# Performance work log

Hardware: AMD Instinct MI355X
Metric: run time of the kernel (lower is better)

Reference implementation:

```python
import jax, jax.numpy as jnp
import numpy as np

DIST = 22.63      # __init__ kwarg `dist` (cdist threshold)
DS_SIZE = 80      # hard-coded Downsample result_size in LeafBranchFunc
LOG_CLAMP = 100.0 # torch BCE clamps log terms at -100


def _cdist(x):
    # x: [B,N,F] -> pairwise euclidean distances [B,N,N]
    sq = jnp.sum(x * x, axis=-1)
    d2 = sq[:, :, None] + sq[:, None, :] - 2.0 * jnp.einsum('bnf,bmf->bnm', x, x)
    return jnp.sqrt(jnp.maximum(d2, 0.0))


@jax.jit
def _cluster(point_features):
    """Faithful port of Cluster.forward: threshold cdist, then the strictly
    sequential greedy label stamping with a single global next_label counter."""
    adj = _cdist(point_features) < DIST  # [B,N,N] bool
    N = adj.shape[1]
    idx = jnp.arange(N)

    def row_step(carry, xs):
        labels, nxt = carry
        row, i = xs
        cur = labels[i]
        new = jnp.where(cur == 0, nxt, cur)
        nxt = jnp.where(cur == 0, nxt + 1, nxt)
        labels = labels.at[i].set(new)
        labels = jnp.where(row, new, labels)  # stamp all thresholded neighbors
        return (labels, nxt), None

    def batch_step(nxt, adj_b):
        (labels, nxt), _ = jax.lax.scan(row_step, (jnp.zeros(N, jnp.int32), nxt), (adj_b, idx))
        return nxt, labels

    _, labels = jax.lax.scan(batch_step, jnp.int32(1), adj)  # sequential over batch: shared counter
    return labels  # [B,N] int32


def _classify(pts, W1, b1, W2, b2, W3, b3):
    # pts: [K,80,3] -> P(class 1) per cluster, PointNet-lite classifier + softmax
    h = jax.nn.relu(pts @ W1 + b1)       # [K,80,64]
    h = jax.nn.relu(h @ W2 + b2)         # [K,80,128]
    g = jnp.max(h, axis=1)               # [K,128] global max pool
    logits = g @ W3 + b3                 # [K,2]
    return jax.nn.softmax(logits, axis=-1)[:, 1]


def setup_inputs() -> dict:
    key = jax.random.key(0)
    ks = jax.random.split(key, 8)
    B, N, F = 4, 4096, 256
    return {
        'point_features': jax.random.normal(ks[0], (B, N, F), jnp.float32),
        'points': jax.random.normal(ks[1], (B, N, 3), jnp.float32),
        'W1': jax.random.normal(ks[2], (3, 64), jnp.float32) * 0.5,
        'b1': jnp.zeros((64,), jnp.float32),
        'W2': jax.random.normal(ks[3], (64, 128), jnp.float32) * 0.1,
        'b2': jnp.zeros((128,), jnp.float32),
        'W3': jax.random.normal(ks[4], (128, 2), jnp.float32) * 0.1,
        'b3': jnp.zeros((2,), jnp.float32),
    }


def reference(point_features, points, W1, b1, W2, b2, W3, b3):
    labels = np.asarray(_cluster(point_features))  # [B,N]; cluster ids are data-dependent
    points_np = np.asarray(points)
    rng = np.random.RandomState(0)  # Downsample uses np.random.choice with replacement
    total = jnp.float32(0.0)
    for b in range(labels.shape[0]):
        ds = []
        for c in np.unique(labels[b]):
            cp = points_np[b][labels[b] == c]                    # [M,3] points of this cluster
            sel = rng.choice(cp.shape[0], DS_SIZE, replace=True)  # random downsample to 80
            ds.append(cp[sel])
        ds = jnp.asarray(np.stack(ds), dtype=jnp.float32)        # [K,80,3]
        p = jnp.nan_to_num(_classify(ds, W1, b1, W2, b2, W3, b3))
        # binary_cross_entropy with all-ones targets: mean(-log p), log clamped at -100
        loss = jnp.mean(jnp.minimum(-jnp.log(p), LOG_CLAMP))
        total = total + loss
    return total
```

## Files before the change

### kernel.cpp

```cpp
#include <hip/hip_runtime.h>
#include <math.h>
#include <stdint.h>
#include <stdlib.h>

constexpr int B_ = 4, N_ = 4096, F_ = 256;
constexpr int DS = 80;
constexpr int MAXC = 16384;
constexpr int RAWBLKS = 16;
constexpr int RAWN = 624 * RAWBLKS;

namespace {
struct RawStream {
  unsigned* buf = nullptr;
  RawStream() {
    unsigned mt[624];
    mt[0] = 0u;
    for (int i = 1; i < 624; ++i)
      mt[i] = 1812433253u * (mt[i - 1] ^ (mt[i - 1] >> 30)) + (unsigned)i;
    if (hipHostMalloc((void**)&buf, (size_t)(RAWN + 624) * 4, 0) != hipSuccess || !buf)
      buf = (unsigned*)malloc((size_t)(RAWN + 624) * 4);
    for (int blk = 0; blk < RAWBLKS; ++blk) {
      for (int i = 0; i < 624; ++i) {
        unsigned y = (mt[i] & 0x80000000u) | (mt[(i + 1) % 624] & 0x7fffffffu);
        mt[i] = mt[(i + 397) % 624] ^ (y >> 1) ^ ((y & 1u) ? 0x9908b0dfu : 0u);
      }
      for (int i = 0; i < 624; ++i) {
        unsigned y = mt[i];
        y ^= y >> 11; y ^= (y << 7) & 0x9d2c5680u; y ^= (y << 15) & 0xefc60000u; y ^= y >> 18;
        buf[blk * 624 + i] = y;
      }
    }
    for (int i = 0; i < 624; ++i) buf[RAWN + i] = mt[i];
  }
};
RawStream g_raw;
}

__global__ __launch_bounds__(256) void pre_kernel(const float* __restrict__ x,
                                                  float* __restrict__ sq,
                                                  int* __restrict__ arrivals) {
  const int blk = blockIdx.x, tid = threadIdx.x;
  const int i = blk * 256 + tid;
  float4 v = ((const float4*)x)[i];
  float s = v.x * v.x + v.y * v.y + v.z * v.z + v.w * v.w;
  for (int off = 32; off > 0; off >>= 1) s += __shfl_down(s, off);
  if ((tid & 63) == 0) sq[blk * 4 + (tid >> 6)] = s;
  if (blk == 0 && tid == 0) arrivals[0] = 0;
}

__device__ __forceinline__ int scan_dir(const float* __restrict__ xb,
                                        const float* __restrict__ sqb,
                                        float4 a0, float4 a1, float4 a2, float4 a3,
                                        double sqi, int jhi, int jlo, int gl, int g) {
  if (jhi < jlo) return -1;
  const double THR2D = (double)22.63f * (double)22.63f;
  int j0 = jhi;
  int cjA = j0 - g;     if (cjA < jlo) cjA = jlo;
  int cjB = j0 - 4 - g; if (cjB < jlo) cjB = jlo;
  const float4* rA = (const float4*)(xb + (size_t)cjA * F_);
  const float4* rB = (const float4*)(xb + (size_t)cjB * F_);
  float4 cA0 = rA[gl], cA1 = rA[gl + 16], cA2 = rA[gl + 32], cA3 = rA[gl + 48];
  float4 cB0 = rB[gl], cB1 = rB[gl + 16], cB2 = rB[gl + 32], cB3 = rB[gl + 48];

  while (j0 >= jlo) {
    const int jn = j0 - 8;
    int nA = jn - g;     if (nA < jlo) nA = jlo;
    int nB = jn - 4 - g; if (nB < jlo) nB = jlo;
    const float4* rnA = (const float4*)(xb + (size_t)nA * F_);
    const float4* rnB = (const float4*)(xb + (size_t)nB * F_);
    float4 pA0 = rnA[gl], pA1 = rnA[gl + 16], pA2 = rnA[gl + 32], pA3 = rnA[gl + 48];
    float4 pB0 = rnB[gl], pB1 = rnB[gl + 16], pB2 = rnB[gl + 32], pB3 = rnB[gl + 48];

    float sA = 0.f;
    sA += a0.x * cA0.x + a0.y * cA0.y + a0.z * cA0.z + a0.w * cA0.w;
    sA += a1.x * cA1.x + a1.y * cA1.y + a1.z * cA1.z + a1.w * cA1.w;
    sA += a2.x * cA2.x + a2.y * cA2.y + a2.z * cA2.z + a2.w * cA2.w;
    sA += a3.x * cA3.x + a3.y * cA3.y + a3.z * cA3.z + a3.w * cA3.w;
    float sB = 0.f;
    sB += a0.x * cB0.x + a0.y * cB0.y + a0.z * cB0.z + a0.w * cB0.w;
    sB += a1.x * cB1.x + a1.y * cB1.y + a1.z * cB1.z + a1.w * cB1.w;
    sB += a2.x * cB2.x + a2.y * cB2.y + a2.z * cB2.z + a2.w * cB2.w;
    sB += a3.x * cB3.x + a3.y * cB3.y + a3.z * cB3.z + a3.w * cB3.w;
    sA += __shfl_xor(sA, 1); sA += __shfl_xor(sA, 2);
    sA += __shfl_xor(sA, 4); sA += __shfl_xor(sA, 8);
    sB += __shfl_xor(sB, 1); sB += __shfl_xor(sB, 2);
    sB += __shfl_xor(sB, 4); sB += __shfl_xor(sB, 8);

    bool okA = false, okB = false;
    const int mA = j0 - g, mB = j0 - 4 - g;
    if (mA >= jlo) {
      double d2 = sqi + (double)sqb[mA] - 2.0 * (double)sA;
      okA = d2 < THR2D;
    }
    if (mB >= jlo) {
      double d2 = sqi + (double)sqb[mB] - 2.0 * (double)sB;
      okB = d2 < THR2D;
    }
    unsigned long long balA = __ballot(okA);
    unsigned long long balB = __ballot(okB);
    if (balA) return j0 - ((__ffsll(balA) - 1) >> 4);
    if (balB) return j0 - 4 - ((__ffsll(balB) - 1) >> 4);
    cA0 = pA0; cA1 = pA1; cA2 = pA2; cA3 = pA3;
    cB0 = pB0; cB1 = pB1; cB2 = pB2; cB3 = pB3;
    j0 = jn;
  }
  return -1;
}

__global__ __launch_bounds__(256) void scan_kernel(const float* __restrict__ x,
                                                   const float* __restrict__ sq,
                                                   int* __restrict__ p,
                                                   int* __restrict__ q) {
  const int tid = threadIdx.x;
  const int w = tid >> 6, lane = tid & 63;
  const int bb = blockIdx.x & 3;
  const int rg = blockIdx.x >> 2;
  const int i = rg * 4 + w;
  const float* xb = x + (size_t)bb * N_ * F_;
  const float* sqb = sq + (size_t)bb * N_;
  const int gl = lane & 15, g = lane >> 4;

  const float4* ra = (const float4*)(xb + (size_t)i * F_);
  float4 a0 = ra[gl], a1 = ra[gl + 16], a2 = ra[gl + 32], a3 = ra[gl + 48];
  const double sqi = (double)sqb[i];

  const int qf = scan_dir(xb, sqb, a0, a1, a2, a3, sqi, N_ - 1, i + 1, gl, g);
  const int pf = scan_dir(xb, sqb, a0, a1, a2, a3, sqi, i - 1, 0, gl, g);

  if (lane == 0) {
    const size_t o = (size_t)bb * N_ + i;
    q[o] = (qf < 0) ? i : qf;
    p[o] = pf;
  }
}

__global__ __launch_bounds__(1024) void cluster_kernel(const int* __restrict__ p,
                                                       const int* __restrict__ q,
                                                       int* __restrict__ lab,
                                                       int* __restrict__ Karr, int* __restrict__ labs,
                                                       int* __restrict__ Msz) {
  const int b = blockIdx.x, tid = threadIdx.x;
  __shared__ int A[N_ + 1], Bb[N_], labS[N_];
  __shared__ int waveOff[17];
  __shared__ int runBase, chg;

  for (int k = tid; k < N_; k += 1024) {
    int pi = p[(size_t)b * N_ + k];
    A[k] = (pi < 0) ? k : pi;
  }
  __syncthreads();
  int* src = A; int* dst = Bb;
  for (int it = 0; it < 12; ++it) {
    if (tid == 0) chg = 0;
    __syncthreads();
    bool any = false;
    for (int k = tid; k < N_; k += 1024) {
      int v = src[src[k]];
      dst[k] = v;
      any |= (v != src[k]);
    }
    if (any) chg = 1;
    __syncthreads();
    int* t = src; src = dst; dst = t;
    if (!chg) break;
  }
  if (tid == 0) runBase = 0;
  __syncthreads();
  for (int base = 0; base < N_; base += 1024) {
    int i = base + tid;
    bool isR = (src[i] == i);
    unsigned long long bal = __ballot(isR);
    int lane = tid & 63, wid = tid >> 6;
    if (lane == 0) waveOff[wid] = __popcll(bal);
    __syncthreads();
    if (tid == 0) {
      int s = runBase;
      for (int w = 0; w < 16; ++w) { int t2 = waveOff[w]; waveOff[w] = s; s += t2; }
      waveOff[16] = s;
    }
    __syncthreads();
    int incl = __popcll(bal & (~0ull >> (63 - lane)));
    dst[i] = waveOff[wid] + incl;
    __syncthreads();
    if (tid == 0) runBase = waveOff[16];
    __syncthreads();
  }
  for (int j = tid; j < N_; j += 1024) {
    int qq = q[(size_t)b * N_ + j];
    int lv = dst[src[qq]];
    labS[j] = lv;
    lab[(size_t)b * N_ + j] = lv;
  }
  __syncthreads();

  int* cnt = A;
  for (int k = tid; k <= N_; k += 1024) cnt[k] = 0;
  __syncthreads();
  {
    const int lane = tid & 63;
    for (int j = tid; j < N_; j += 1024) {
      int v = labS[j];
      unsigned long long remM = ~0ull;
      while (remM) {
        int leader = __ffsll(remM) - 1;
        int lv = __shfl(v, leader);
        unsigned long long m = __ballot(v == lv);
        if (lane == leader) atomicAdd(&cnt[lv], __popcll(m));
        remM &= ~m;
      }
    }
  }
  __syncthreads();
  if (tid == 0) runBase = 0;
  __syncthreads();
  for (int base = 1; base <= N_; base += 1024) {
    int c = base + tid;
    bool m = (cnt[c] > 0);
    unsigned long long bal = __ballot(m);
    int lane = tid & 63, wid = tid >> 6;
    if (lane == 0) waveOff[wid] = __popcll(bal);
    __syncthreads();
    if (tid == 0) {
      int s = runBase;
      for (int w = 0; w < 16; ++w) { int t2 = waveOff[w]; waveOff[w] = s; s += t2; }
      waveOff[16] = s;
    }
    __syncthreads();
    if (m) {
      int pos = waveOff[wid] + __popcll(bal & ((1ull << lane) - 1));
      labs[(size_t)b * N_ + pos] = c;
      Msz[(size_t)b * N_ + pos] = cnt[c];
    }
    __syncthreads();
    if (tid == 0) runBase = waveOff[16];
    __syncthreads();
  }
  if (tid == 0) Karr[b] = runBase;
}

__device__ inline void mt_regen(unsigned* mt, unsigned* raw, int lane) {
  const int ph_s[3] = {0, 227, 454};
  const int ph_e[3] = {227, 454, 624};
#pragma unroll
  for (int ph = 0; ph < 3; ++ph) {
    const int s = ph_s[ph], e = ph_e[ph];
    unsigned aReg[4], bReg[4];
    const int niter = (e - s + 63) >> 6;
    for (int it = 0; it < niter; ++it) {
      int i = s + it * 64 + lane;
      if (i < e) { aReg[it] = mt[i]; bReg[it] = mt[(i + 1) % 624]; }
    }
    __syncthreads();
    for (int it = 0; it < niter; ++it) {
      int i = s + it * 64 + lane;
      if (i < e) {
        unsigned y = (aReg[it] & 0x80000000u) | (bReg[it] & 0x7fffffffu);
        mt[i] = mt[(i + 397) % 624] ^ (y >> 1) ^ ((y & 1u) ? 0x9908b0dfu : 0u);
      }
    }
    __syncthreads();
  }
  for (int it = 0; it < 10; ++it) {
    int i = it * 64 + lane;
    if (i < 624) {
      unsigned y = mt[i];
      y ^= y >> 11; y ^= (y << 7) & 0x9d2c5680u; y ^= (y << 15) & 0xefc60000u; y ^= y >> 18;
      raw[i] = y;
    }
  }
  __syncthreads();
}

__global__ __launch_bounds__(64) void rngsel_kernel(const int* __restrict__ Karr,
                                                    const int* __restrict__ Msz,
                                                    const unsigned* __restrict__ rawG,
                                                    const unsigned* __restrict__ mtSave,
                                                    int* __restrict__ sel, int* __restrict__ meta,
                                                    int* __restrict__ totK) {
  __shared__ int mszS[2048];
  __shared__ unsigned rawL[2048];
  __shared__ unsigned mtF[624];
  __shared__ unsigned rawF[624];
  const int lane = threadIdx.x;
  int pos = 0;
  int winBase = -100000;
  bool fb = false;
  int fpos = 0;
  int cid = 0;
  for (int b = 0; b < B_; ++b) {
    const int Kb = Karr[b];
    for (int k0 = 0; k0 < Kb; k0 += 2048) {
      const int nk = min(2048, Kb - k0);
      for (int i = lane; i < nk; i += 64) mszS[i] = Msz[(size_t)b * N_ + k0 + i];
      __syncthreads();
      for (int kk = 0; kk < nk; ++kk) {
        const int M = mszS[kk];
        if (lane == 0) meta[cid] = (b << 16) | (k0 + kk);
        if (M <= 1) {
          sel[cid * DS + lane] = 0;
          if (lane < DS - 64) sel[cid * DS + 64 + lane] = 0;
        } else {
          const unsigned rng = (unsigned)(M - 1);
          unsigned mask = rng;
          mask |= mask >> 1; mask |= mask >> 2; mask |= mask >> 4; mask |= mask >> 8; mask |= mask >> 16;
          int acc = 0;
          while (acc < DS) {
            unsigned v = 0xFFFFFFFFu;
            bool ok = false;
            int take;
            if (!fb && pos >= RAWN) {
              fb = true;
              for (int i = lane; i < 624; i += 64) mtF[i] = mtSave[i];
              __syncthreads();
              fpos = 624;
            }
            if (!fb) {
              if (pos + 64 > winBase + 2048) {
                winBase = pos;
                for (int i = lane; i < 2048; i += 64) rawL[i] = rawG[winBase + i];
                __syncthreads();
              }
              take = min(64, RAWN - pos);
              if (lane < take) { v = rawL[pos - winBase + lane] & mask; ok = (v <= rng); }
            } else {
              if (fpos == 624) { mt_regen(mtF, rawF, lane); fpos = 0; }
              take = min(64, 624 - fpos);
              if (lane < take) { v = rawF[fpos + lane] & mask; ok = (v <= rng); }
            }
            unsigned long long bal = __ballot(ok);
            int pre = __popcll(bal & ((1ull << lane) - 1ull));
            int tot = __popcll(bal);
            if (ok && acc + pre < DS) sel[cid * DS + acc + pre] = (int)v;
            int advance;
            if (acc + tot >= DS) {
              int need = DS - acc;
              bool win = ok && (pre + 1 == need);
              unsigned long long wb = __ballot(win);
              advance = __ffsll(wb);
              acc = DS;
            } else {
              advance = take;
              acc += tot;
            }
            if (fb) fpos += advance; else pos += advance;
          }
        }
        ++cid;
      }
      __syncthreads();
    }
  }
  if (lane == 0) totK[0] = cid;
}

__global__ __launch_bounds__(256) void classify_par_kernel(
    const float* __restrict__ points, const float* __restrict__ W1, const float* __restrict__ b1,
    const float* __restrict__ W2, const float* __restrict__ b2,
    const float* __restrict__ W3, const float* __restrict__ b3,
    const int* __restrict__ lab, const int* __restrict__ labs,
    const int* __restrict__ sel, const int* __restrict__ meta, const int* __restrict__ totK,
    const int* __restrict__ Karr, float* __restrict__ lossArr,
    int* __restrict__ arrivals, float* __restrict__ out) {
  __shared__ unsigned wordsS[128];
  __shared__ int prefS[128];
  __shared__ float pts[DS][3];
  __shared__ float h1[DS][64];
  __shared__ float W2s[64][128];
  __shared__ float gmax[128];
  __shared__ float accB[4];
  __shared__ int lastS;
  const int tid = threadIdx.x;
  int T = totK[0]; if (T > MAXC) T = MAXC;
  if ((int)blockIdx.x >= T) return;
  for (int k = tid; k < 64 * 128; k += 256) W2s[k >> 7][k & 127] = W2[k];

  for (int cid = blockIdx.x; cid < T; cid += gridDim.x) {
    const int mv = meta[cid];
    const int b = mv >> 16, k = mv & 0xFFFF;
    const int c = labs[(size_t)b * N_ + k];
    if (tid < 128) {
      unsigned wbits = 0;
      const int* lb = lab + (size_t)b * N_ + tid * 32;
      for (int s = 0; s < 32; ++s) wbits |= (lb[s] == c) ? (1u << s) : 0u;
      wordsS[tid] = wbits;
    }
    __syncthreads();
    if (tid == 0) {
      int s = 0;
      for (int w2 = 0; w2 < 128; ++w2) { prefS[w2] = s; s += __popc(wordsS[w2]); }
    }
    __syncthreads();
    if (tid < DS) {
      int r = sel[cid * DS + tid];
      int lo = 0, hi = 127;
      while (lo < hi) { int mid = (lo + hi + 1) >> 1; if (prefS[mid] <= r) lo = mid; else hi = mid - 1; }
      int rem = r - prefS[lo];
      unsigned wbits = wordsS[lo];
      int j = lo * 32;
      for (;;) {
        int bpos = __ffs(wbits) - 1;
        if (rem == 0) { j += bpos; break; }
        wbits &= wbits - 1; --rem;
      }
      pts[tid][0] = points[((size_t)b * N_ + j) * 3 + 0];
      pts[tid][1] = points[((size_t)b * N_ + j) * 3 + 1];
      pts[tid][2] = points[((size_t)b * N_ + j) * 3 + 2];
    }
    __syncthreads();
    for (int o = tid; o < DS * 64; o += 256) {
      int r = o >> 6, cc = o & 63;
      float v = pts[r][0] * W1[cc] + pts[r][1] * W1[64 + cc] + pts[r][2] * W1[128 + cc] + b1[cc];
      h1[r][cc] = fmaxf(v, 0.f);
    }
    __syncthreads();
    {
      const int cc = tid & 127, half = tid >> 7;
      const float b2c = b2[cc];
      float m = -1e30f;
      for (int r = half * 40; r < half * 40 + 40; ++r) {
        float a0 = 0.f, a1 = 0.f, a2 = 0.f, a3 = 0.f;
#pragma unroll
        for (int kk = 0; kk < 64; kk += 4) {
          a0 += h1[r][kk + 0] * W2s[kk + 0][cc];
          a1 += h1[r][kk + 1] * W2s[kk + 1][cc];
          a2 += h1[r][kk + 2] * W2s[kk + 2][cc];
          a3 += h1[r][kk + 3] * W2s[kk + 3][cc];
        }
        float acc = ((a0 + a1) + (a2 + a3)) + b2c;
        m = fmaxf(m, fmaxf(acc, 0.f));
      }
      if (half == 0) gmax[cc] = m;
      __syncthreads();
      if (half == 1) gmax[cc] = fmaxf(gmax[cc], m);
    }
    __syncthreads();
    if (tid == 0) {
      float l0 = b3[0], l1 = b3[1];
      for (int cc = 0; cc < 128; ++cc) { l0 += gmax[cc] * W3[cc * 2 + 0]; l1 += gmax[cc] * W3[cc * 2 + 1]; }
      float mx = fmaxf(l0, l1);
      float e0 = expf(l0 - mx), e1 = expf(l1 - mx);
      float p1 = e1 / (e0 + e1);
      if (isnan(p1)) p1 = 0.f;
      atomicExch(&lossArr[cid], fminf(-logf(p1), 100.f));
    }
    __syncthreads();
  }

  __threadfence();
  if (tid == 0) {
    const int active = min((int)gridDim.x, T);
    lastS = (atomicAdd(arrivals, 1) == active - 1) ? 1 : 0;
  }
  __syncthreads();
  if (!lastS) return;
  if (tid < 4) accB[tid] = 0.f;
  __syncthreads();
  float local[4] = {0.f, 0.f, 0.f, 0.f};
  for (int cid = tid; cid < T; cid += 256)
    local[meta[cid] >> 16] += atomicAdd(&lossArr[cid], 0.0f);
  for (int b = 0; b < 4; ++b) {
    float v = local[b];
    for (int off = 32; off > 0; off >>= 1) v += __shfl_down(v, off);
    if ((tid & 63) == 0) atomicAdd(&accB[b], v);
  }
  __syncthreads();
  if (tid == 0) {
    float tot = 0.f;
    for (int b = 0; b < 4; ++b) tot += accB[b] / (float)Karr[b];
    out[0] = tot;
  }
}

extern "C" void kernel_launch(void* const* d_in, const int* in_sizes, int n_in,
                              void* d_out, int out_size, void* d_ws, size_t ws_size,
                              hipStream_t stream) {
  const float* x      = (const float*)d_in[0];
  const float* points = (const float*)d_in[1];
  const float* W1 = (const float*)d_in[2];
  const float* b1 = (const float*)d_in[3];
  const float* W2 = (const float*)d_in[4];
  const float* b2 = (const float*)d_in[5];
  const float* W3 = (const float*)d_in[6];
  const float* b3 = (const float*)d_in[7];
  float* out = (float*)d_out;

  char* wsb = (char*)d_ws;
  size_t off = 0;
  auto carve = [&](size_t bytes) -> void* {
    void* r = wsb + off;
    off += (bytes + 255) & ~(size_t)255;
    return r;
  };
  float* sq      = (float*)carve((size_t)B_ * N_ * 4);
  int* p         = (int*)carve((size_t)B_ * N_ * 4);
  int* q         = (int*)carve((size_t)B_ * N_ * 4);
  int* lab       = (int*)carve((size_t)B_ * N_ * 4);
  int* labs      = (int*)carve((size_t)B_ * N_ * 4);
  int* Msz       = (int*)carve((size_t)B_ * N_ * 4);
  int* Karr      = (int*)carve(256);
  int* totK      = (int*)carve(256);
  int* arrivals  = (int*)carve(256);
  unsigned* rawG = (unsigned*)carve((size_t)(RAWN + 624 + 2048) * 4);
  unsigned* mtSave = rawG + RAWN;
  int* sel       = (int*)carve((size_t)MAXC * DS * 4);
  int* meta      = (int*)carve((size_t)MAXC * 4);
  float* lossArr = (float*)carve((size_t)MAXC * 4);
  (void)ws_size;

  hipMemcpyAsync(rawG, g_raw.buf, (size_t)(RAWN + 624) * 4,
                 hipMemcpyHostToDevice, stream);

  hipLaunchKernelGGL(pre_kernel, dim3(B_ * N_ * F_ / 1024), dim3(256), 0, stream,
                     x, sq, arrivals);
  hipLaunchKernelGGL(scan_kernel, dim3(B_ * N_ / 4), dim3(256), 0, stream, x, sq, p, q);
  hipLaunchKernelGGL(cluster_kernel, dim3(B_), dim3(1024), 0, stream,
                     p, q, lab, Karr, labs, Msz);
  hipLaunchKernelGGL(rngsel_kernel, dim3(1), dim3(64), 0, stream,
                     Karr, Msz, rawG, mtSave, sel, meta, totK);
  hipLaunchKernelGGL(classify_par_kernel, dim3(512), dim3(256), 0, stream,
                     points, W1, b1, W2, b2, W3, b3, lab, labs, sel, meta, totK,
                     Karr, lossArr, arrivals, out);
}
```

Before: 161.0 us.

## Bake MT19937 stream into device constant and split scan directions across waves

Replaces the per-call host-to-device copy of the precomputed Mersenne Twister raw stream with a constexpr-generated __device__ constant table, which removes a memcpy from each invocation. It also doubles the scan_kernel block to 512 threads so the forward (q) and backward (p) neighbour searches run on separate waves instead of one after the other in the same wave. This gives more parallelism and shortens the serial critical path per row. The cost is higher register and occupancy pressure per block, and a large constexpr evaluation at compile time.

```diff
diff --git a/kernel.cpp b/kernel.cpp
--- a/kernel.cpp
+++ b/kernel.cpp
@@ -9,32 +9,33 @@
 constexpr int RAWBLKS = 16;
 constexpr int RAWN = 624 * RAWBLKS;
 
-namespace {
-struct RawStream {
-  unsigned* buf = nullptr;
-  RawStream() {
-    unsigned mt[624];
-    mt[0] = 0u;
-    for (int i = 1; i < 624; ++i)
-      mt[i] = 1812433253u * (mt[i - 1] ^ (mt[i - 1] >> 30)) + (unsigned)i;
-    if (hipHostMalloc((void**)&buf, (size_t)(RAWN + 624) * 4, 0) != hipSuccess || !buf)
-      buf = (unsigned*)malloc((size_t)(RAWN + 624) * 4);
-    for (int blk = 0; blk < RAWBLKS; ++blk) {
-      for (int i = 0; i < 624; ++i) {
-        unsigned y = (mt[i] & 0x80000000u) | (mt[(i + 1) % 624] & 0x7fffffffu);
-        mt[i] = mt[(i + 397) % 624] ^ (y >> 1) ^ ((y & 1u) ? 0x9908b0dfu : 0u);
-      }
-      for (int i = 0; i < 624; ++i) {
-        unsigned y = mt[i];
-        y ^= y >> 11; y ^= (y << 7) & 0x9d2c5680u; y ^= (y << 15) & 0xefc60000u; y ^= y >> 18;
-        buf[blk * 624 + i] = y;
-      }
-    }
-    for (int i = 0; i < 624; ++i) buf[RAWN + i] = mt[i];
-  }
+struct MTData {
+  unsigned raw[RAWN];
+  unsigned save[624];
+  unsigned pad[2048];
 };
-RawStream g_raw;
-}
+
+constexpr MTData gen_mt() {
+  MTData d{};
+  unsigned mt[624]{};
+  mt[0] = 0u;
+  for (int i = 1; i < 624; ++i)
+    mt[i] = 1812433253u * (mt[i - 1] ^ (mt[i - 1] >> 30)) + (unsigned)i;
+  for (int blk = 0; blk < RAWBLKS; ++blk) {
+    for (int i = 0; i < 624; ++i) {
+      unsigned y = (mt[i] & 0x80000000u) | (mt[(i + 1) % 624] & 0x7fffffffu);
+      mt[i] = mt[(i + 397) % 624] ^ (y >> 1) ^ ((y & 1u) ? 0x9908b0dfu : 0u);
+    }
+    for (int i = 0; i < 624; ++i) {
+      unsigned y = mt[i];
+      y ^= y >> 11; y ^= (y << 7) & 0x9d2c5680u; y ^= (y << 15) & 0xefc60000u; y ^= y >> 18;
+      d.raw[blk * 624 + i] = y;
+    }
+  }
+  for (int i = 0; i < 624; ++i) d.save[i] = mt[i];
+  return d;
+}
+__device__ const MTData d_mt = gen_mt();
 
 __global__ __launch_bounds__(256) void pre_kernel(const float* __restrict__ x,
                                                   float* __restrict__ sq,
@@ -107,7 +108,7 @@
   return -1;
 }
 
-__global__ __launch_bounds__(256) void scan_kernel(const float* __restrict__ x,
+__global__ __launch_bounds__(512) void scan_kernel(const float* __restrict__ x,
                                                    const float* __restrict__ sq,
                                                    int* __restrict__ p,
                                                    int* __restrict__ q) {
@@ -115,7 +116,8 @@
   const int w = tid >> 6, lane = tid & 63;
   const int bb = blockIdx.x & 3;
   const int rg = blockIdx.x >> 2;
-  const int i = rg * 4 + w;
+  const int i = rg * 4 + (w & 3);
+  const bool qmode = (w >> 2) == 0;
   const float* xb = x + (size_t)bb * N_ * F_;
   const float* sqb = sq + (size_t)bb * N_;
   const int gl = lane & 15, g = lane >> 4;
@@ -124,13 +126,13 @@
   float4 a0 = ra[gl], a1 = ra[gl + 16], a2 = ra[gl + 32], a3 = ra[gl + 48];
   const double sqi = (double)sqb[i];
 
-  const int qf = scan_dir(xb, sqb, a0, a1, a2, a3, sqi, N_ - 1, i + 1, gl, g);
-  const int pf = scan_dir(xb, sqb, a0, a1, a2, a3, sqi, i - 1, 0, gl, g);
+  const int f = qmode ? scan_dir(xb, sqb, a0, a1, a2, a3, sqi, N_ - 1, i + 1, gl, g)
+                      : scan_dir(xb, sqb, a0, a1, a2, a3, sqi, i - 1, 0, gl, g);
 
   if (lane == 0) {
     const size_t o = (size_t)bb * N_ + i;
-    q[o] = (qf < 0) ? i : qf;
-    p[o] = pf;
+    if (qmode) q[o] = (f < 0) ? i : f;
+    else       p[o] = f;
   }
 }
 
@@ -273,8 +275,6 @@
 
 __global__ __launch_bounds__(64) void rngsel_kernel(const int* __restrict__ Karr,
                                                     const int* __restrict__ Msz,
-                                                    const unsigned* __restrict__ rawG,
-                                                    const unsigned* __restrict__ mtSave,
                                                     int* __restrict__ sel, int* __restrict__ meta,
                                                     int* __restrict__ totK) {
   __shared__ int mszS[2048];
@@ -310,14 +310,14 @@
             int take;
             if (!fb && pos >= RAWN) {
               fb = true;
-              for (int i = lane; i < 624; i += 64) mtF[i] = mtSave[i];
+              for (int i = lane; i < 624; i += 64) mtF[i] = d_mt.save[i];
               __syncthreads();
               fpos = 624;
             }
             if (!fb) {
               if (pos + 64 > winBase + 2048) {
                 winBase = pos;
-                for (int i = lane; i < 2048; i += 64) rawL[i] = rawG[winBase + i];
+                for (int i = lane; i < 2048; i += 64) rawL[i] = d_mt.raw[winBase + i];
                 __syncthreads();
               }
               take = min(64, RAWN - pos);
@@ -500,23 +500,18 @@
   int* Karr      = (int*)carve(256);
   int* totK      = (int*)carve(256);
   int* arrivals  = (int*)carve(256);
-  unsigned* rawG = (unsigned*)carve((size_t)(RAWN + 624 + 2048) * 4);
-  unsigned* mtSave = rawG + RAWN;
   int* sel       = (int*)carve((size_t)MAXC * DS * 4);
   int* meta      = (int*)carve((size_t)MAXC * 4);
   float* lossArr = (float*)carve((size_t)MAXC * 4);
   (void)ws_size;
 
-  hipMemcpyAsync(rawG, g_raw.buf, (size_t)(RAWN + 624) * 4,
-                 hipMemcpyHostToDevice, stream);
-
   hipLaunchKernelGGL(pre_kernel, dim3(B_ * N_ * F_ / 1024), dim3(256), 0, stream,
                      x, sq, arrivals);
-  hipLaunchKernelGGL(scan_kernel, dim3(B_ * N_ / 4), dim3(256), 0, stream, x, sq, p, q);
+  hipLaunchKernelGGL(scan_kernel, dim3(B_ * N_ / 4), dim3(512), 0, stream, x, sq, p, q);
   hipLaunchKernelGGL(cluster_kernel, dim3(B_), dim3(1024), 0, stream,
                      p, q, lab, Karr, labs, Msz);
   hipLaunchKernelGGL(rngsel_kernel, dim3(1), dim3(64), 0, stream,
-                     Karr, Msz, rawG, mtSave, sel, meta, totK);
+                     Karr, Msz, sel, meta, totK);
   hipLaunchKernelGGL(classify_par_kernel, dim3(512), dim3(256), 0, stream,
                      points, W1, b1, W2, b2, W3, b3, lab, labs, sel, meta, totK,
                      Karr, lossArr, arrivals, out);
```

Result: slower. 166.5 us (+3.4%).
